# Optimization experiments

Measured on AMD Instinct MI355X. Metric: run time of the kernel, lower is better.

## Reference

```python
import jax, jax.numpy as jnp
import numpy as np

N = 20000      # nodes per snapshot
E = 160000     # edges per snapshot
T = 8          # timesteps
F_IN = 256     # nfeat
HEADS = 4      # GAT heads
C = 128        # nhid_graph (per-head GAT out, concat=False -> mean)
GH = 128       # nhid_gru
NC = 2         # nclass
NEG_SLOPE = 0.2


def setup_inputs() -> dict:
    key = jax.random.key(0)
    ks = jax.random.split(key, 16)
    s = 0.05
    return {
        "graph": jax.random.randint(ks[0], (T, 2, E), 0, N),
        "fts": jax.random.normal(ks[1], (T, N, F_IN), dtype=jnp.float32),
        "time_steps": T,
        # GATConv params (PyG-style): lin weight, att_src/att_dst, bias
        "W_gat": jax.random.normal(ks[2], (F_IN, HEADS * C), dtype=jnp.float32) * s,
        "att_src": jax.random.normal(ks[3], (HEADS, C), dtype=jnp.float32) * s,
        "att_dst": jax.random.normal(ks[4], (HEADS, C), dtype=jnp.float32) * s,
        "b_gat": jax.random.normal(ks[5], (C,), dtype=jnp.float32) * s,
        # GRU params (torch layout: [3H, in], gates order r,z,n)
        "W_ih": jax.random.normal(ks[6], (3 * GH, C), dtype=jnp.float32) * s,
        "W_hh": jax.random.normal(ks[7], (3 * GH, GH), dtype=jnp.float32) * s,
        "b_ih": jax.random.normal(ks[8], (3 * GH,), dtype=jnp.float32) * s,
        "b_hh": jax.random.normal(ks[9], (3 * GH,), dtype=jnp.float32) * s,
        # Attention ('general'): linear_in [H,H] no bias, linear_out [H,2H] no bias
        "W_att_in": jax.random.normal(ks[10], (GH, GH), dtype=jnp.float32) * s,
        "W_att_out": jax.random.normal(ks[11], (GH, 2 * GH), dtype=jnp.float32) * s,
        # final classifier
        "W_cls": jax.random.normal(ks[12], (NC, GH), dtype=jnp.float32) * s,
        "b_cls": jax.random.normal(ks[13], (NC,), dtype=jnp.float32) * s,
    }


def _segment_softmax(logits, seg, num_segments):
    # logits: [E', H], seg: [E'] destination node ids
    m = jax.ops.segment_max(logits, seg, num_segments=num_segments)
    m = jnp.where(jnp.isfinite(m), m, 0.0)
    e = jnp.exp(logits - m[seg])
    s = jax.ops.segment_sum(e, seg, num_segments=num_segments)
    return e / (s[seg] + 1e-16)


def _gat_step(x, edge_index, W_gat, att_src, att_dst, b_gat):
    # PyG GATConv: concat=False (mean over heads), negative_slope=0.2,
    # add_self_loops=True; eval mode so attention dropout is identity.
    n = x.shape[0]
    xw = (x @ W_gat).reshape(n, HEADS, C)                 # [N,H,C]
    loops = jnp.arange(n, dtype=edge_index.dtype)
    src = jnp.concatenate([edge_index[0], loops])         # [E']
    dst = jnp.concatenate([edge_index[1], loops])
    a_src = jnp.einsum('nhc,hc->nh', xw, att_src)         # [N,H]
    a_dst = jnp.einsum('nhc,hc->nh', xw, att_dst)
    alpha = jax.nn.leaky_relu(a_src[src] + a_dst[dst], NEG_SLOPE)  # [E',H]
    alpha = _segment_softmax(alpha, dst, n)
    msg = xw[src] * alpha[..., None]                      # [E',H,C]
    out = jax.ops.segment_sum(msg, dst, num_segments=n)   # [N,H,C]
    return out.mean(axis=1) + b_gat                       # [N,C]


def _gru(y, W_ih, W_hh, b_ih, b_hh):
    # y: [T, N, C]; torch GRU equations, h0 = 0
    n = y.shape[1]
    def step(h, x):
        gi = x @ W_ih.T + b_ih
        gh = h @ W_hh.T + b_hh
        i_r, i_z, i_n = jnp.split(gi, 3, axis=-1)
        h_r, h_z, h_n = jnp.split(gh, 3, axis=-1)
        r = jax.nn.sigmoid(i_r + h_r)
        z = jax.nn.sigmoid(i_z + h_z)
        nn_ = jnp.tanh(i_n + r * h_n)
        h_new = (1.0 - z) * nn_ + z * h
        return h_new, h_new
    h0 = jnp.zeros((n, GH), dtype=y.dtype)
    last, full = jax.lax.scan(step, h0, y)
    return full, last  # [T,N,GH], [N,GH]


def reference(graph, fts, time_steps, W_gat, att_src, att_dst, b_gat,
              W_ih, W_hh, b_ih, b_hh, W_att_in, W_att_out, W_cls, b_cls):
    # per-timestep GAT + leaky_relu(0.2)
    ys = [jax.nn.leaky_relu(
            _gat_step(fts[i], graph[i], W_gat, att_src, att_dst, b_gat),
            NEG_SLOPE)
          for i in range(time_steps)]
    y = jnp.stack(ys)                                     # [T,N,C]
    context, last = _gru(y, W_ih, W_hh, b_ih, b_hh)
    query = last[:, None, :]                              # [N,1,GH]
    context = jnp.transpose(context, (1, 0, 2))           # [N,T,GH]
    # Attention('general')
    q = query @ W_att_in.T                                # [N,1,GH]
    scores = jnp.einsum('nod,ntd->not', q, context)       # [N,1,T]
    w = jax.nn.softmax(scores, axis=-1)
    mix = jnp.einsum('not,ntd->nod', w, context)          # [N,1,GH]
    combined = jnp.concatenate([mix, q], axis=-1)         # [N,1,2GH]
    att_out = jnp.tanh(combined @ W_att_out.T)            # [N,1,GH]
    output = jax.nn.leaky_relu(att_out.reshape(-1, GH), NEG_SLOPE)
    logits = output @ W_cls.T + b_cls                     # [N,NC]
    return jax.nn.log_softmax(logits, axis=1)
```

## Files before the change

kernel.cpp:

```cpp
#include <hip/hip_runtime.h>
#include <hip/hip_bf16.h>
#include <math.h>

#define N_NODES 20000
#define N_EDGES 160000
#define T_STEPS 8
#define F_INC   256
#define HEADS   4
#define CCH     128
#define KC      512
#define GHD     128
#define G3      384
#define SLOPE   0.2f
#define SEG     (N_EDGES + N_NODES)
#define TN      (T_STEPS * N_NODES)
#define SCAN_BLKS ((TN + 1023) / 1024)

typedef unsigned short u16;
typedef __attribute__((ext_vector_type(8))) short bf16x8;
typedef __attribute__((ext_vector_type(4))) float f32x4;

__device__ __forceinline__ float leakyf(float x) { return x > 0.f ? x : SLOPE * x; }
__device__ __forceinline__ float b2f(u16 u) {
  union { unsigned int i; float f; } x; x.i = ((unsigned int)u) << 16; return x.f;
}
__device__ __forceinline__ u16 f2b(float f) {
  union { float f; unsigned int i; } u; u.f = f;
  unsigned int r = u.i + 0x7FFFu + ((u.i >> 16) & 1u);
  return (u16)(r >> 16);
}
__device__ __forceinline__ float sigf(float x) { return 1.f / (1.f + expf(-x)); }

__device__ __forceinline__ void gload16(const void* g, void* l) {
  __builtin_amdgcn_global_load_lds(
      (const __attribute__((address_space(1))) unsigned int*)g,
      (__attribute__((address_space(3))) unsigned int*)l, 16, 0, 0);
}

__device__ __forceinline__ bf16x8 cvt8(f32x4 lo, f32x4 hi) {
  union { unsigned int u[4]; bf16x8 v; } r;
  asm("v_cvt_pk_bf16_f32 %0, %1, %2" : "=v"(r.u[0]) : "v"(lo[0]), "v"(lo[1]));
  asm("v_cvt_pk_bf16_f32 %0, %1, %2" : "=v"(r.u[1]) : "v"(lo[2]), "v"(lo[3]));
  asm("v_cvt_pk_bf16_f32 %0, %1, %2" : "=v"(r.u[2]) : "v"(hi[0]), "v"(hi[1]));
  asm("v_cvt_pk_bf16_f32 %0, %1, %2" : "=v"(r.u[3]) : "v"(hi[2]), "v"(hi[3]));
  return r.v;
}

template <int OBF, int FUSE, int AFP32>
__global__ __launch_bounds__(256) void gemm_bf16(
    const void* __restrict__ Ain, const u16* __restrict__ B,
    const float* __restrict__ bias, void* __restrict__ Cout,
    int M, int K, int Nt, int swz,
    const float* __restrict__ attS, const float* __restrict__ attD,
    float* __restrict__ asrc, float* __restrict__ adst)
{
  __shared__ __align__(16) char AsRaw[128 * 32 * 4];
  __shared__ u16 Bs[128][32];
  __shared__ float s_as[128], s_ad[128];
  float* AsF = (float*)AsRaw;
  u16 (*Asb)[32] = (u16(*)[32])AsRaw;
  const int tid  = threadIdx.x;
  const int wave = tid >> 6, lane = tid & 63;
  const int wr = (wave >> 1) * 64, wc = (wave & 1) * 64;
  int bx = blockIdx.x, by = blockIdx.y;
  if (swz) {
    const int gx = gridDim.x;
    const int nwg = gx * (int)gridDim.y;
    const int lin = by * gx + bx;
    const int q = nwg >> 3, r = nwg & 7;
    const int xcd = lin & 7, idx = lin >> 3;
    const int wg = (xcd < r ? xcd * (q + 1) : r * (q + 1) + (xcd - r) * q) + idx;
    bx = wg % gx; by = wg / gx;
  }
  const int bm = by * 128, bn = bx * 128;
  const int l15 = lane & 15, g = lane >> 4;

  if (FUSE && tid < 128) { s_as[tid] = 0.f; s_ad[tid] = 0.f; }

  const int sr = tid >> 2, sd = tid & 3;
  const int ss = sd ^ ((sr >> 1) & 3);
  const u16* aS0 = 0; const u16* aS1 = 0; u16* lA0 = 0; u16* lA1 = 0;
  const float* aF[4]; float* lAF[4];
  if (AFP32) {
    const float* Af = (const float*)Ain;
    const int row0 = tid >> 3, sd8 = tid & 7;
    const int ss8 = sd8 ^ (row0 & 7);
    #pragma unroll
    for (int p = 0; p < 4; ++p) {
      int row = row0 + p * 32;
      aF[p] = Af + (size_t)min(bm + row, M - 1) * K + ss8 * 4;
      lAF[p] = AsF + (size_t)(p * 256 + (tid & ~63)) * 4;
    }
  } else {
    const u16* Ab = (const u16*)Ain;
    aS0 = Ab + (size_t)min(bm + sr,      M - 1) * K + ss * 8;
    aS1 = Ab + (size_t)min(bm + 64 + sr, M - 1) * K + ss * 8;
    lA0 = (u16*)AsRaw + (size_t)(tid & ~63) * 8;
    lA1 = lA0 + 2048;
  }
  const u16* bS0 = B + (size_t)(bn + sr)      * K + ss * 8;
  const u16* bS1 = B + (size_t)(bn + 64 + sr) * K + ss * 8;
  u16* lB0 = &Bs[0][0] + (size_t)(tid & ~63) * 8;
  u16* lB1 = lB0 + 2048;

  f32x4 acc[4][4];
  #pragma unroll
  for (int m = 0; m < 4; ++m)
    #pragma unroll
    for (int n = 0; n < 4; ++n)
      #pragma unroll
      for (int j = 0; j < 4; ++j) acc[m][n][j] = 0.f;

  const int nK = K >> 5;
  for (int kt = 0; kt < nK; ++kt) {
    const int ko = kt * 32;
    if (AFP32) {
      #pragma unroll
      for (int p = 0; p < 4; ++p) gload16(aF[p] + ko, lAF[p]);
    } else {
      gload16(aS0 + ko, lA0);
      gload16(aS1 + ko, lA1);
    }
    gload16(bS0 + ko, lB0);
    gload16(bS1 + ko, lB1);
    __syncthreads();
    bf16x8 af[4], bfr[4];
    #pragma unroll
    for (int m = 0; m < 4; ++m) {
      int row = wr + m * 16 + l15;
      if (AFP32) {
        int s0 = (2 * g) ^ (row & 7), s1 = (2 * g + 1) ^ (row & 7);
        f32x4 lo = *(const f32x4*)&AsF[row * 32 + s0 * 4];
        f32x4 hi = *(const f32x4*)&AsF[row * 32 + s1 * 4];
        af[m] = cvt8(lo, hi);
      } else {
        af[m] = *(const bf16x8*)&Asb[row][(g ^ ((row >> 1) & 3)) * 8];
      }
      int rowb = wc + m * 16 + l15;
      bfr[m] = *(const bf16x8*)&Bs[rowb][(g ^ ((rowb >> 1) & 3)) * 8];
    }
    #pragma unroll
    for (int m = 0; m < 4; ++m)
      #pragma unroll
      for (int n = 0; n < 4; ++n)
        acc[m][n] = __builtin_amdgcn_mfma_f32_16x16x32_bf16(af[m], bfr[n], acc[m][n], 0, 0, 0);
    __syncthreads();
  }
  if (FUSE != 2) {
    #pragma unroll
    for (int m = 0; m < 4; ++m) {
      int row0 = bm + wr + m * 16 + g * 4;
      #pragma unroll
      for (int n = 0; n < 4; ++n) {
        int col = bn + wc + n * 16 + l15;
        float bv = bias ? bias[col] : 0.f;
        #pragma unroll
        for (int j = 0; j < 4; ++j) {
          int row = row0 + j;
          if (row < M) {
            float v = acc[m][n][j] + bv;
            if (OBF) ((u16*)Cout)[(size_t)row * Nt + col] = f2b(v);
            else     ((float*)Cout)[(size_t)row * Nt + col] = v;
          }
        }
      }
    }
  }
  if (FUSE) {
    float ps[4][4], pd[4][4];
    #pragma unroll
    for (int m = 0; m < 4; ++m)
      #pragma unroll
      for (int j = 0; j < 4; ++j) { ps[m][j] = 0.f; pd[m][j] = 0.f; }
    #pragma unroll
    for (int n = 0; n < 4; ++n) {
      int cl = wc + n * 16 + l15;
      float wsv = attS[bn + cl], wdv = attD[bn + cl];
      #pragma unroll
      for (int m = 0; m < 4; ++m)
        #pragma unroll
        for (int j = 0; j < 4; ++j) {
          float av = acc[m][n][j];
          if (FUSE == 2) av = leakyf(tanhf(av));
          ps[m][j] = fmaf(av, wsv, ps[m][j]);
          pd[m][j] = fmaf(av, wdv, pd[m][j]);
        }
    }
    #pragma unroll
    for (int m = 0; m < 4; ++m)
      #pragma unroll
      for (int j = 0; j < 4; ++j)
        #pragma unroll
        for (int msk = 8; msk >= 1; msk >>= 1) {
          ps[m][j] += __shfl_xor(ps[m][j], msk);
          pd[m][j] += __shfl_xor(pd[m][j], msk);
        }
    if (l15 == 0) {
      #pragma unroll
      for (int m = 0; m < 4; ++m)
        #pragma unroll
        for (int j = 0; j < 4; ++j) {
          atomicAdd(&s_as[wr + m * 16 + g * 4 + j], ps[m][j]);
          atomicAdd(&s_ad[wr + m * 16 + g * 4 + j], pd[m][j]);
        }
    }
    __syncthreads();
    if (tid < 128) {
      int row = bm + tid;
      if (row < M) {
        if (FUSE == 1) {
          int h = bn >> 7;
          asrc[(size_t)row * 4 + h] = s_as[tid];
          adst[(size_t)row * 4 + h] = s_ad[tid];
        } else {
          float l0 = s_as[tid] + bias[0];
          float l1 = s_ad[tid] + bias[1];
          float mx = fmaxf(l0, l1);
          float lse = mx + logf(expf(l0 - mx) + expf(l1 - mx));
          asrc[(size_t)row * 2 + 0] = l0 - lse;
          asrc[(size_t)row * 2 + 1] = l1 - lse;
        }
      }
    }
  }
}

__global__ void convert_weights(const float* __restrict__ w_ih, const float* __restrict__ w_hh,
                                const float* __restrict__ w_in, const float* __restrict__ w_out,
                                u16* __restrict__ wihb, u16* __restrict__ whhb,
                                u16* __restrict__ winb, u16* __restrict__ woutb)
{
  int i = blockIdx.x * 256 + threadIdx.x;
  const float* src; u16* dst; int base;
  if      (i < 6144)  { src = w_ih;  dst = wihb;  base = i; }
  else if (i < 12288) { src = w_hh;  dst = whhb;  base = i - 6144; }
  else if (i < 14336) { src = w_in;  dst = winb;  base = i - 12288; }
  else                { src = w_out; dst = woutb; base = i - 14336; }
  int o = base * 8;
  float4 v0 = *(const float4*)(src + o);
  float4 v1 = *(const float4*)(src + o + 4);
  bf16x8 ov;
  ov[0] = (short)f2b(v0.x); ov[1] = (short)f2b(v0.y);
  ov[2] = (short)f2b(v0.z); ov[3] = (short)f2b(v0.w);
  ov[4] = (short)f2b(v1.x); ov[5] = (short)f2b(v1.y);
  ov[6] = (short)f2b(v1.z); ov[7] = (short)f2b(v1.w);
  *(bf16x8*)(dst + o) = ov;
}

__global__ void conv_transpose_wgat(const float* __restrict__ src, u16* __restrict__ dst) {
  int idx = blockIdx.x * 256 + threadIdx.x;
  if (idx >= KC * F_INC) return;
  int n = idx >> 8, k = idx & 255;
  dst[(size_t)n * F_INC + k] = f2b(src[(size_t)k * KC + n]);
}

__global__ void count_kernel(const int* __restrict__ graph, int* __restrict__ counts) {
  int e = blockIdx.x * 256 + threadIdx.x;
  int t = blockIdx.y;
  if (e < N_EDGES) {
    int d = graph[(size_t)t * 2 * N_EDGES + N_EDGES + e];
    atomicAdd(&counts[t * N_NODES + d], 1);
  }
}

__global__ __launch_bounds__(1024) void scanA(
    const int* __restrict__ counts, int* __restrict__ offs, int* __restrict__ bsums)
{
  const int tid = threadIdx.x, lane = tid & 63, w = tid >> 6;
  __shared__ int s_wt[16];
  int i = blockIdx.x * 1024 + tid;
  int v = (i < TN) ? (counts[i] + 1) : 0;
  int x = v;
  #pragma unroll
  for (int d = 1; d < 64; d <<= 1) {
    int nvl = __shfl_up(x, d, 64);
    if (lane >= d) x += nvl;
  }
  if (lane == 63) s_wt[w] = x;
  __syncthreads();
  if (tid < 16) {
    int y = s_wt[tid];
    #pragma unroll
    for (int d = 1; d < 16; d <<= 1) {
      int nvl = __shfl_up(y, d, 64);
      if (tid >= d) y += nvl;
    }
    s_wt[tid] = y;
  }
  __syncthreads();
  int wbase = (w > 0) ? s_wt[w - 1] : 0;
  if (i < TN) offs[i] = wbase + x - v;
  if (tid == 1023) bsums[blockIdx.x] = s_wt[15];
}

__global__ void scanB(int* __restrict__ bsums, int* __restrict__ offs) {
  const int lane = threadIdx.x;
  int carry = 0;
  for (int base = 0; base < 192; base += 64) {
    int idx = base + lane;
    int v = (idx < SCAN_BLKS) ? bsums[idx] : 0;
    int x = v;
    #pragma unroll
    for (int d = 1; d < 64; d <<= 1) {
      int nvl = __shfl_up(x, d, 64);
      if (lane >= d) x += nvl;
    }
    if (idx < SCAN_BLKS) bsums[idx] = carry + x - v;
    carry += __shfl(x, 63);
  }
  if (lane == 0) offs[TN] = carry;
}

__global__ __launch_bounds__(1024) void scanC(int* __restrict__ offs, const int* __restrict__ bsums) {
  int i = blockIdx.x * 1024 + threadIdx.x;
  if (i < TN) offs[i] += bsums[blockIdx.x];
}

__global__ void scatter_kernel(const int* __restrict__ graph, const int* __restrict__ offs,
                               int* __restrict__ cursor, int* __restrict__ ssrc)
{
  int i = blockIdx.x * 256 + threadIdx.x;
  int t = blockIdx.y;
  if (i >= SEG) return;
  int s, d;
  if (i < N_EDGES) {
    s = graph[(size_t)t * 2 * N_EDGES + i];
    d = graph[(size_t)t * 2 * N_EDGES + N_EDGES + i];
  } else {
    s = d = i - N_EDGES;
  }
  int pos = offs[t * N_NODES + d] + atomicAdd(&cursor[t * N_NODES + d], 1);
  ssrc[pos] = s;
}

__global__ __launch_bounds__(256) void aggregate_kernel(
    const u16* __restrict__ xw, const float* __restrict__ a_src,
    const float* __restrict__ a_dst, const float* __restrict__ b_gat,
    const int* __restrict__ offs, const int* __restrict__ ssrc,
    u16* __restrict__ yout)
{
  const int wv = threadIdx.x >> 6, lane = threadIdx.x & 63;
  const int nd = blockIdx.x * 4 + wv;
  const int t  = blockIdx.y;
  const int ob = t * N_NODES + nd;
  const int beg = offs[ob], end = offs[ob + 1];
  const size_t rowbase = (size_t)t * N_NODES;
  const int he   = lane & 3;
  const int eidx = lane >> 2;
  const int hl   = lane >> 4;
  const float advh = a_dst[(rowbase + nd) * 4 + he];

  float m = -INFINITY, ssum = 0.f;
  float acc[8] = {0.f,0.f,0.f,0.f,0.f,0.f,0.f,0.f};

#define FMA8(W, X)                                                        \
    { float _w = (W);                                                     \
      acc[0] = fmaf(_w, __uint_as_float((unsigned)(X).x << 16), acc[0]);  \
      acc[1] = fmaf(_w, __uint_as_float((unsigned)(X).x & 0xffff0000u), acc[1]); \
      acc[2] = fmaf(_w, __uint_as_float((unsigned)(X).y << 16), acc[2]);  \
      acc[3] = fmaf(_w, __uint_as_float((unsigned)(X).y & 0xffff0000u), acc[3]); \
      acc[4] = fmaf(_w, __uint_as_float((unsigned)(X).z << 16), acc[4]);  \
      acc[5] = fmaf(_w, __uint_as_float((unsigned)(X).z & 0xffff0000u), acc[5]); \
      acc[6] = fmaf(_w, __uint_as_float((unsigned)(X).w << 16), acc[6]);  \
      acc[7] = fmaf(_w, __uint_as_float((unsigned)(X).w & 0xffff0000u), acc[7]); }
#define LDE(SVAR) (*(const int4*)&xw[(rowbase + (SVAR)) * KC + lane * 8])

  for (int base = beg; base < end; base += 16) {
    const int cnt = min(16, end - base);
    const int e = base + eidx;
    const int sidx = (e < end) ? ssrc[e] : ssrc[base];
    const float av = a_src[(rowbase + sidx) * 4 + he];
    const float a = (eidx < cnt) ? leakyf(av + advh) : -INFINITY;
    float cm = a;
    cm = fmaxf(cm, __shfl_xor(cm, 4));
    cm = fmaxf(cm, __shfl_xor(cm, 8));
    cm = fmaxf(cm, __shfl_xor(cm, 16));
    cm = fmaxf(cm, __shfl_xor(cm, 32));
    const float nm = fmaxf(m, cm);
    const float sc = expf(m - nm);
    const float w = expf(a - nm);
    float ts = w;
    ts += __shfl_xor(ts, 4);
    ts += __shfl_xor(ts, 8);
    ts += __shfl_xor(ts, 16);
    ts += __shfl_xor(ts, 32);
    ssum = ssum * sc + ts;
    m = nm;
    const float schl = __shfl(sc, hl);
    #pragma unroll
    for (int k = 0; k < 8; ++k) acc[k] *= schl;

    const int cpad = (cnt + 3) & ~3;
    int b4 = 0;
    for (; b4 + 8 <= cpad; b4 += 8) {
      const int s0 = __shfl(sidx, (b4 + 0) << 2);
      const int s1 = __shfl(sidx, (b4 + 1) << 2);
      const int s2 = __shfl(sidx, (b4 + 2) << 2);
      const int s3 = __shfl(sidx, (b4 + 3) << 2);
      const int s4 = __shfl(sidx, (b4 + 4) << 2);
      const int s5 = __shfl(sidx, (b4 + 5) << 2);
      const int s6 = __shfl(sidx, (b4 + 6) << 2);
      const int s7 = __shfl(sidx, (b4 + 7) << 2);
      const int4 x0 = LDE(s0); const int4 x1 = LDE(s1);
      const int4 x2 = LDE(s2); const int4 x3 = LDE(s3);
      const int4 x4 = LDE(s4); const int4 x5 = LDE(s5);
      const int4 x6 = LDE(s6); const int4 x7 = LDE(s7);
      const float w0 = __shfl(w, ((b4 + 0) << 2) + hl);
      const float w1 = __shfl(w, ((b4 + 1) << 2) + hl);
      const float w2 = __shfl(w, ((b4 + 2) << 2) + hl);
      const float w3 = __shfl(w, ((b4 + 3) << 2) + hl);
      const float w4 = __shfl(w, ((b4 + 4) << 2) + hl);
      const float w5 = __shfl(w, ((b4 + 5) << 2) + hl);
      const float w6 = __shfl(w, ((b4 + 6) << 2) + hl);
      const float w7 = __shfl(w, ((b4 + 7) << 2) + hl);
      FMA8(w0, x0); FMA8(w1, x1); FMA8(w2, x2); FMA8(w3, x3);
      FMA8(w4, x4); FMA8(w5, x5); FMA8(w6, x6); FMA8(w7, x7);
    }
    if (b4 < cpad) {
      const int s0 = __shfl(sidx, (b4 + 0) << 2);
      const int s1 = __shfl(sidx, (b4 + 1) << 2);
      const int s2 = __shfl(sidx, (b4 + 2) << 2);
      const int s3 = __shfl(sidx, (b4 + 3) << 2);
      const int4 x0 = LDE(s0); const int4 x1 = LDE(s1);
      const int4 x2 = LDE(s2); const int4 x3 = LDE(s3);
      const float w0 = __shfl(w, ((b4 + 0) << 2) + hl);
      const float w1 = __shfl(w, ((b4 + 1) << 2) + hl);
      const float w2 = __shfl(w, ((b4 + 2) << 2) + hl);
      const float w3 = __shfl(w, ((b4 + 3) << 2) + hl);
      FMA8(w0, x0); FMA8(w1, x1); FMA8(w2, x2); FMA8(w3, x3);
    }
  }
#undef LDE
#undef FMA8

  const float sh = __shfl(ssum, hl);
  const float inv = 1.f / (sh + 1e-16f);
  #pragma unroll
  for (int k = 0; k < 8; ++k) {
    acc[k] *= inv;
    acc[k] += __shfl_xor(acc[k], 16);
    acc[k] += __shfl_xor(acc[k], 32);
  }
  if (lane < 16) {
    bf16x8 ov;
    #pragma unroll
    for (int k = 0; k < 8; ++k) {
      float v = acc[k] * 0.25f + b_gat[lane * 8 + k];
      ov[k] = (short)f2b(leakyf(v));
    }
    *(bf16x8*)&yout[(rowbase + nd) * GHD + lane * 8] = ov;
  }
}

__global__ __launch_bounds__(256) void gru_seq(
    const u16* __restrict__ Whh, const float* __restrict__ b_hh,
    const u16* __restrict__ giall, u16* __restrict__ ctx)
{
  __shared__ u16 hA[32][128];
  __shared__ u16 reg2[12288];
  u16 (*Bs)[32] = (u16(*)[32])reg2;
  const int tid = threadIdx.x, lane = tid & 63, wv = tid >> 6;
  const int l15 = lane & 15, g = lane >> 4;
  const int bm = blockIdx.x * 32;

  const int sr = tid >> 2, sd = tid & 3;
  const int ssb = sd ^ ((sr >> 1) & 3);
  const u16* bS[6]; u16* lB[6];
  #pragma unroll
  for (int p = 0; p < 6; ++p) {
    bS[p] = Whh + (size_t)(sr + p * 64) * GHD + ssb * 8;
    lB[p] = reg2 + (size_t)(p * 256 + (tid & ~63)) * 8;
  }
  float bbv[6];
  #pragma unroll
  for (int n = 0; n < 6; ++n) bbv[n] = b_hh[wv * 96 + n * 16 + l15];

  const int cr = tid >> 3;
  const int cg = (tid & 7) * 8;
  const int grow = bm + cr;
  const size_t gb = (size_t)grow * G3;
  const size_t cb = (size_t)grow * GHD;
  float hp[2][8];

  #pragma unroll
  for (int q = 0; q < 2; ++q) {
    const int c0 = cg + q * 64;
    bf16x8 ir8 = *(const bf16x8*)&giall[gb + c0];
    bf16x8 iz8 = *(const bf16x8*)&giall[gb + 128 + c0];
    bf16x8 in8 = *(const bf16x8*)&giall[gb + 256 + c0];
    float4 br0 = *(const float4*)&b_hh[c0];       float4 br1 = *(const float4*)&b_hh[c0 + 4];
    float4 bz0 = *(const float4*)&b_hh[128 + c0]; float4 bz1 = *(const float4*)&b_hh[128 + c0 + 4];
    float4 bn0 = *(const float4*)&b_hh[256 + c0]; float4 bn1 = *(const float4*)&b_hh[256 + c0 + 4];
    float bhr[8] = {br0.x, br0.y, br0.z, br0.w, br1.x, br1.y, br1.z, br1.w};
    float bhz[8] = {bz0.x, bz0.y, bz0.z, bz0.w, bz1.x, bz1.y, bz1.z, bz1.w};
    float bhn[8] = {bn0.x, bn0.y, bn0.z, bn0.w, bn1.x, bn1.y, bn1.z, bn1.w};
    bf16x8 hv;
    #pragma unroll
    for (int k = 0; k < 8; ++k) {
      float rr = sigf(b2f((u16)ir8[k]) + bhr[k]);
      float zz = sigf(b2f((u16)iz8[k]) + bhz[k]);
      float nn = tanhf(b2f((u16)in8[k]) + rr * bhn[k]);
      float h = (1.f - zz) * nn;
      hp[q][k] = h;
      hv[k] = (short)f2b(h);
    }
    const int sl = (c0 >> 3) ^ (cr & 7);
    *(bf16x8*)&hA[cr][sl * 8] = hv;
    *(bf16x8*)&ctx[cb + c0] = hv;
  }
  __syncthreads();

  for (int t = 1; t < T_STEPS; ++t) {
    const u16* gi_t = giall + (size_t)t * N_NODES * G3;
    u16* ctx_t = ctx + (size_t)t * N_NODES * GHD;
    f32x4 acc[2][6];
    #pragma unroll
    for (int m = 0; m < 2; ++m)
      #pragma unroll
      for (int n = 0; n < 6; ++n)
        #pragma unroll
        for (int j = 0; j < 4; ++j) acc[m][n][j] = 0.f;

    #pragma unroll
    for (int kt = 0; kt < 4; ++kt) {
      const int ko = kt * 32;
      #pragma unroll
      for (int p = 0; p < 6; ++p) gload16(bS[p] + ko, lB[p]);
      __syncthreads();
      bf16x8 af[2], bfr[6];
      #pragma unroll
      for (int m = 0; m < 2; ++m) {
        int row = m * 16 + l15;
        int sl = (kt * 4 + g) ^ (row & 7);
        af[m] = *(const bf16x8*)&hA[row][sl * 8];
      }
      #pragma unroll
      for (int n = 0; n < 6; ++n) {
        int rowb = wv * 96 + n * 16 + l15;
        bfr[n] = *(const bf16x8*)&Bs[rowb][(g ^ ((rowb >> 1) & 3)) * 8];
      }
      #pragma unroll
      for (int m = 0; m < 2; ++m)
        #pragma unroll
        for (int n = 0; n < 6; ++n)
          acc[m][n] = __builtin_amdgcn_mfma_f32_16x16x32_bf16(af[m], bfr[n], acc[m][n], 0, 0, 0);
      __syncthreads();
    }
    #pragma unroll
    for (int m = 0; m < 2; ++m)
      #pragma unroll
      for (int n = 0; n < 6; ++n) {
        int c = wv * 96 + n * 16 + l15;
        #pragma unroll
        for (int j = 0; j < 4; ++j) {
          int r = m * 16 + g * 4 + j;
          reg2[r * 384 + (((c >> 3) ^ (r & 7)) << 3) + (c & 7)] = f2b(acc[m][n][j] + bbv[n]);
        }
      }
    __syncthreads();
    #pragma unroll
    for (int q = 0; q < 2; ++q) {
      const int c0 = cg + q * 64;
      const int sl0 = ((c0 >> 3) ^ (cr & 7));
      const int sl1 = (((128 + c0) >> 3) ^ (cr & 7));
      const int sl2 = (((256 + c0) >> 3) ^ (cr & 7));
      bf16x8 hr8 = *(bf16x8*)&reg2[cr * 384 + sl0 * 8];
      bf16x8 hz8 = *(bf16x8*)&reg2[cr * 384 + sl1 * 8];
      bf16x8 hn8 = *(bf16x8*)&reg2[cr * 384 + sl2 * 8];
      bf16x8 ir8 = *(const bf16x8*)&gi_t[gb + c0];
      bf16x8 iz8 = *(const bf16x8*)&gi_t[gb + 128 + c0];
      bf16x8 in8 = *(const bf16x8*)&gi_t[gb + 256 + c0];
      bf16x8 hv;
      #pragma unroll
      for (int k = 0; k < 8; ++k) {
        float rr = sigf(b2f((u16)ir8[k]) + b2f((u16)hr8[k]));
        float zz = sigf(b2f((u16)iz8[k]) + b2f((u16)hz8[k]));
        float nn = tanhf(b2f((u16)in8[k]) + rr * b2f((u16)hn8[k]));
        float h = (1.f - zz) * nn + zz * hp[q][k];
        hp[q][k] = h;
        hv[k] = (short)f2b(h);
      }
      const int slh = (c0 >> 3) ^ (cr & 7);
      *(bf16x8*)&hA[cr][slh * 8] = hv;
      *(bf16x8*)&ctx_t[cb + c0] = hv;
    }
    __syncthreads();
  }
}

__global__ __launch_bounds__(256) void attn_mid(
    const u16* __restrict__ ctx, const float* __restrict__ q,
    u16* __restrict__ comb)
{
  const int node = blockIdx.x * 4 + (threadIdx.x >> 6);
  const int lane = threadIdx.x & 63;
  if (node >= N_NODES) return;
  const float q0 = q[(size_t)node * GHD + lane];
  const float q1 = q[(size_t)node * GHD + 64 + lane];
  float c0[T_STEPS], c1[T_STEPS], w[T_STEPS];
  float mx = -1e30f;
  #pragma unroll
  for (int t = 0; t < T_STEPS; ++t) {
    const u16* cr = ctx + ((size_t)t * N_NODES + node) * GHD;
    c0[t] = b2f(cr[lane]); c1[t] = b2f(cr[64 + lane]);
    float p = q0 * c0[t] + q1 * c1[t];
    #pragma unroll
    for (int m = 32; m >= 1; m >>= 1) p += __shfl_xor(p, m);
    w[t] = p;
    mx = fmaxf(mx, p);
  }
  float s = 0.f;
  #pragma unroll
  for (int t = 0; t < T_STEPS; ++t) { w[t] = expf(w[t] - mx); s += w[t]; }
  const float inv = 1.f / s;
  float m0 = 0.f, m1 = 0.f;
  #pragma unroll
  for (int t = 0; t < T_STEPS; ++t) { m0 = fmaf(w[t], c0[t], m0); m1 = fmaf(w[t], c1[t], m1); }
  m0 *= inv; m1 *= inv;
  u16* cb = comb + (size_t)node * 2 * GHD;
  cb[lane]       = f2b(m0);
  cb[64 + lane]  = f2b(m1);
  cb[128 + lane] = f2b(q0);
  cb[192 + lane] = f2b(q1);
}

extern "C" void kernel_launch(void* const* d_in, const int* in_sizes, int n_in,
                              void* d_out, int out_size, void* d_ws, size_t ws_size,
                              hipStream_t stream)
{
  const int*   graph     = (const int*)  d_in[0];
  const float* fts       = (const float*)d_in[1];
  const float* W_gat     = (const float*)d_in[3];
  const float* att_src   = (const float*)d_in[4];
  const float* att_dst   = (const float*)d_in[5];
  const float* b_gat     = (const float*)d_in[6];
  const float* W_ih      = (const float*)d_in[7];
  const float* W_hh      = (const float*)d_in[8];
  const float* b_ih      = (const float*)d_in[9];
  const float* b_hh      = (const float*)d_in[10];
  const float* W_att_in  = (const float*)d_in[11];
  const float* W_att_out = (const float*)d_in[12];
  const float* W_cls     = (const float*)d_in[13];
  const float* b_cls     = (const float*)d_in[14];
  float* out = (float*)d_out;

  char* ws = (char*)d_ws;
  size_t off = 0;
  auto alloc = [&](size_t bytes) {
    void* p = ws + off;
    off = (off + bytes + 255) & ~(size_t)255;
    return p;
  };
  const size_t NT = (size_t)TN;
  u16*   wgatT = (u16*)alloc((size_t)KC * F_INC * 2);
  u16*   wihb  = (u16*)alloc((size_t)G3 * GHD * 2);
  u16*   whhb  = (u16*)alloc((size_t)G3 * GHD * 2);
  u16*   winb  = (u16*)alloc((size_t)GHD * GHD * 2);
  u16*   woutb = (u16*)alloc((size_t)GHD * 2 * GHD * 2);
  u16*   xw    = (u16*)alloc(NT * KC * 2);
  float* asrc  = (float*)alloc(NT * 4 * 4);
  float* adst  = (float*)alloc(NT * 4 * 4);
  u16*   yall  = (u16*)alloc(NT * GHD * 2);
  u16*   giall = (u16*)alloc(NT * G3 * 2);
  u16*   ctx   = (u16*)alloc(NT * GHD * 2);
  float* qf    = (float*)alloc((size_t)N_NODES * GHD * 4);
  u16*   comb  = (u16*)alloc((size_t)N_NODES * 2 * GHD * 2);
  int* counts  = (int*)alloc((size_t)2 * TN * 4);
  int* cursor  = counts + TN;
  int* offs    = (int*)alloc((size_t)(TN + 1) * 4);
  int* bsums   = (int*)alloc((size_t)256 * 4);
  int* ssrc    = (int*)alloc((size_t)T_STEPS * SEG * 4);

  conv_transpose_wgat<<<dim3((KC * F_INC + 255) / 256), 256, 0, stream>>>(W_gat, wgatT);
  convert_weights<<<dim3(72), 256, 0, stream>>>(W_ih, W_hh, W_att_in, W_att_out,
                                                wihb, whhb, winb, woutb);

  hipMemsetAsync(counts, 0, (size_t)2 * TN * 4, stream);
  count_kernel<<<dim3(N_EDGES / 256, T_STEPS), 256, 0, stream>>>(graph, counts);
  scanA<<<dim3(SCAN_BLKS), 1024, 0, stream>>>(counts, offs, bsums);
  scanB<<<dim3(1), 64, 0, stream>>>(bsums, offs);
  scanC<<<dim3(SCAN_BLKS), 1024, 0, stream>>>(offs, bsums);
  scatter_kernel<<<dim3((SEG + 255) / 256, T_STEPS), 256, 0, stream>>>(graph, offs, cursor, ssrc);

  gemm_bf16<1, 1, 1><<<dim3(KC / 128, (int)(NT / 128)), 256, 0, stream>>>(
      fts, wgatT, nullptr, xw, (int)NT, F_INC, KC, 1, att_src, att_dst, asrc, adst);

  aggregate_kernel<<<dim3(N_NODES / 4, T_STEPS), 256, 0, stream>>>(
      xw, asrc, adst, b_gat, offs, ssrc, yall);

  gemm_bf16<1, 0, 0><<<dim3(G3 / 128, (int)(NT / 128)), 256, 0, stream>>>(
      yall, wihb, b_ih, giall, (int)NT, GHD, G3, 1, nullptr, nullptr, nullptr, nullptr);

  gru_seq<<<dim3(N_NODES / 32), 256, 0, stream>>>(whhb, b_hh, giall, ctx);

  gemm_bf16<0, 0, 0><<<dim3(1, (N_NODES + 127) / 128), 256, 0, stream>>>(
      ctx + (size_t)(T_STEPS - 1) * N_NODES * GHD, winb, nullptr, qf,
      N_NODES, GHD, GHD, 0, nullptr, nullptr, nullptr, nullptr);
  attn_mid<<<dim3(N_NODES / 4), 256, 0, stream>>>(ctx, qf, comb);
  gemm_bf16<0, 2, 0><<<dim3(1, (N_NODES + 127) / 128), 256, 0, stream>>>(
      comb, woutb, b_cls, nullptr, N_NODES, 2 * GHD, GHD, 0,
      W_cls, W_cls + GHD, out, nullptr);
}
```

Measured before the change: 724.6 us.

## Fuse query projection into GRU kernel, merge weight conversions, pack aggregate FMAs

Computes the attention query projection (last hidden state times W_att_in) inside the GRU kernel epilogue, using the final hidden tile still held in LDS. This removes a separate GEMM launch and the reload of the last context slice, and stores q as bf16 instead of fp32. The two weight conversion kernels are merged into one launch. The aggregate kernel's accumulators become float2 vectors so the compiler can emit packed FMA. The bf16 q adds slight rounding, and the fused epilogue reuses shared buffers, so correctness depends on that LDS state being valid.

```diff
diff --git a/kernel.cpp b/kernel.cpp
--- a/kernel.cpp
+++ b/kernel.cpp
@@ -19,6 +19,7 @@
 typedef unsigned short u16;
 typedef __attribute__((ext_vector_type(8))) short bf16x8;
 typedef __attribute__((ext_vector_type(4))) float f32x4;
+typedef __attribute__((ext_vector_type(2))) float f32x2;
 
 __device__ __forceinline__ float leakyf(float x) { return x > 0.f ? x : SLOPE * x; }
 __device__ __forceinline__ float b2f(u16 u) {
@@ -225,12 +226,21 @@
   }
 }
 
-__global__ void convert_weights(const float* __restrict__ w_ih, const float* __restrict__ w_hh,
-                                const float* __restrict__ w_in, const float* __restrict__ w_out,
-                                u16* __restrict__ wihb, u16* __restrict__ whhb,
-                                u16* __restrict__ winb, u16* __restrict__ woutb)
+__global__ void convert_all(const float* __restrict__ w_gat,
+                            const float* __restrict__ w_ih, const float* __restrict__ w_hh,
+                            const float* __restrict__ w_in, const float* __restrict__ w_out,
+                            u16* __restrict__ wgatT,
+                            u16* __restrict__ wihb, u16* __restrict__ whhb,
+                            u16* __restrict__ winb, u16* __restrict__ woutb)
 {
-  int i = blockIdx.x * 256 + threadIdx.x;
+  int b = blockIdx.x;
+  if (b < 512) {
+    int idx = b * 256 + threadIdx.x;
+    int n = idx >> 8, k = idx & 255;
+    wgatT[(size_t)n * F_INC + k] = f2b(w_gat[(size_t)k * KC + n]);
+    return;
+  }
+  int i = (b - 512) * 256 + threadIdx.x;
   const float* src; u16* dst; int base;
   if      (i < 6144)  { src = w_ih;  dst = wihb;  base = i; }
   else if (i < 12288) { src = w_hh;  dst = whhb;  base = i - 6144; }
@@ -245,13 +255,6 @@
   ov[4] = (short)f2b(v1.x); ov[5] = (short)f2b(v1.y);
   ov[6] = (short)f2b(v1.z); ov[7] = (short)f2b(v1.w);
   *(bf16x8*)(dst + o) = ov;
-}
-
-__global__ void conv_transpose_wgat(const float* __restrict__ src, u16* __restrict__ dst) {
-  int idx = blockIdx.x * 256 + threadIdx.x;
-  if (idx >= KC * F_INC) return;
-  int n = idx >> 8, k = idx & 255;
-  dst[(size_t)n * F_INC + k] = f2b(src[(size_t)k * KC + n]);
 }
 
 __global__ void count_kernel(const int* __restrict__ graph, int* __restrict__ counts) {
@@ -351,18 +354,25 @@
   const float advh = a_dst[(rowbase + nd) * 4 + he];
 
   float m = -INFINITY, ssum = 0.f;
-  float acc[8] = {0.f,0.f,0.f,0.f,0.f,0.f,0.f,0.f};
+  f32x2 acc2[4];
+  #pragma unroll
+  for (int j = 0; j < 4; ++j) { acc2[j][0] = 0.f; acc2[j][1] = 0.f; }
 
 #define FMA8(W, X)                                                        \
-    { float _w = (W);                                                     \
-      acc[0] = fmaf(_w, __uint_as_float((unsigned)(X).x << 16), acc[0]);  \
-      acc[1] = fmaf(_w, __uint_as_float((unsigned)(X).x & 0xffff0000u), acc[1]); \
-      acc[2] = fmaf(_w, __uint_as_float((unsigned)(X).y << 16), acc[2]);  \
-      acc[3] = fmaf(_w, __uint_as_float((unsigned)(X).y & 0xffff0000u), acc[3]); \
-      acc[4] = fmaf(_w, __uint_as_float((unsigned)(X).z << 16), acc[4]);  \
-      acc[5] = fmaf(_w, __uint_as_float((unsigned)(X).z & 0xffff0000u), acc[5]); \
-      acc[6] = fmaf(_w, __uint_as_float((unsigned)(X).w << 16), acc[6]);  \
-      acc[7] = fmaf(_w, __uint_as_float((unsigned)(X).w & 0xffff0000u), acc[7]); }
+    { f32x2 _w2; _w2[0] = (W); _w2[1] = _w2[0];                           \
+      f32x2 _v;                                                           \
+      _v[0] = __uint_as_float((unsigned)(X).x << 16);                     \
+      _v[1] = __uint_as_float((unsigned)(X).x & 0xffff0000u);             \
+      acc2[0] += _w2 * _v;                                                \
+      _v[0] = __uint_as_float((unsigned)(X).y << 16);                     \
+      _v[1] = __uint_as_float((unsigned)(X).y & 0xffff0000u);             \
+      acc2[1] += _w2 * _v;                                                \
+      _v[0] = __uint_as_float((unsigned)(X).z << 16);                     \
+      _v[1] = __uint_as_float((unsigned)(X).z & 0xffff0000u);             \
+      acc2[2] += _w2 * _v;                                                \
+      _v[0] = __uint_as_float((unsigned)(X).w << 16);                     \
+      _v[1] = __uint_as_float((unsigned)(X).w & 0xffff0000u);             \
+      acc2[3] += _w2 * _v; }
 #define LDE(SVAR) (*(const int4*)&xw[(rowbase + (SVAR)) * KC + lane * 8])
 
   for (int base = beg; base < end; base += 16) {
@@ -386,9 +396,12 @@
     ts += __shfl_xor(ts, 32);
     ssum = ssum * sc + ts;
     m = nm;
-    const float schl = __shfl(sc, hl);
-    #pragma unroll
-    for (int k = 0; k < 8; ++k) acc[k] *= schl;
+    {
+      const float schl = __shfl(sc, hl);
+      f32x2 sc2; sc2[0] = schl; sc2[1] = schl;
+      #pragma unroll
+      for (int j = 0; j < 4; ++j) acc2[j] *= sc2;
+    }
 
     const int cpad = (cnt + 3) & ~3;
     int b4 = 0;
@@ -435,9 +448,10 @@
 
   const float sh = __shfl(ssum, hl);
   const float inv = 1.f / (sh + 1e-16f);
+  float acc[8];
   #pragma unroll
   for (int k = 0; k < 8; ++k) {
-    acc[k] *= inv;
+    acc[k] = acc2[k >> 1][k & 1] * inv;
     acc[k] += __shfl_xor(acc[k], 16);
     acc[k] += __shfl_xor(acc[k], 32);
   }
@@ -453,8 +467,9 @@
 }
 
 __global__ __launch_bounds__(256) void gru_seq(
-    const u16* __restrict__ Whh, const float* __restrict__ b_hh,
-    const u16* __restrict__ giall, u16* __restrict__ ctx)
+    const u16* __restrict__ Whh, const u16* __restrict__ Win,
+    const float* __restrict__ b_hh, const u16* __restrict__ giall,
+    u16* __restrict__ ctx, u16* __restrict__ qb)
 {
   __shared__ u16 hA[32][128];
   __shared__ u16 reg2[12288];
@@ -586,17 +601,70 @@
     }
     __syncthreads();
   }
+
+  {
+    const u16* qS[2]; u16* lQ[2];
+    #pragma unroll
+    for (int p = 0; p < 2; ++p) {
+      qS[p] = Win + (size_t)(sr + p * 64) * GHD + ssb * 8;
+      lQ[p] = reg2 + (size_t)(p * 256 + (tid & ~63)) * 8;
+    }
+    f32x4 accq[2][2];
+    #pragma unroll
+    for (int m = 0; m < 2; ++m)
+      #pragma unroll
+      for (int n = 0; n < 2; ++n)
+        #pragma unroll
+        for (int j = 0; j < 4; ++j) accq[m][n][j] = 0.f;
+
+    #pragma unroll
+    for (int kt = 0; kt < 4; ++kt) {
+      const int ko = kt * 32;
+      #pragma unroll
+      for (int p = 0; p < 2; ++p) gload16(qS[p] + ko, lQ[p]);
+      __syncthreads();
+      bf16x8 af[2], bq[2];
+      #pragma unroll
+      for (int m = 0; m < 2; ++m) {
+        int row = m * 16 + l15;
+        int sl = (kt * 4 + g) ^ (row & 7);
+        af[m] = *(const bf16x8*)&hA[row][sl * 8];
+      }
+      #pragma unroll
+      for (int n = 0; n < 2; ++n) {
+        int rowb = wv * 32 + n * 16 + l15;
+        bq[n] = *(const bf16x8*)&Bs[rowb][(g ^ ((rowb >> 1) & 3)) * 8];
+      }
+      #pragma unroll
+      for (int m = 0; m < 2; ++m)
+        #pragma unroll
+        for (int n = 0; n < 2; ++n)
+          accq[m][n] = __builtin_amdgcn_mfma_f32_16x16x32_bf16(af[m], bq[n], accq[m][n], 0, 0, 0);
+      __syncthreads();
+    }
+    #pragma unroll
+    for (int m = 0; m < 2; ++m) {
+      int row0 = bm + m * 16 + g * 4;
+      #pragma unroll
+      for (int n = 0; n < 2; ++n) {
+        int col = wv * 32 + n * 16 + l15;
+        #pragma unroll
+        for (int j = 0; j < 4; ++j)
+          qb[(size_t)(row0 + j) * GHD + col] = f2b(accq[m][n][j]);
+      }
+    }
+  }
 }
 
 __global__ __launch_bounds__(256) void attn_mid(
-    const u16* __restrict__ ctx, const float* __restrict__ q,
+    const u16* __restrict__ ctx, const u16* __restrict__ qb,
     u16* __restrict__ comb)
 {
   const int node = blockIdx.x * 4 + (threadIdx.x >> 6);
   const int lane = threadIdx.x & 63;
   if (node >= N_NODES) return;
-  const float q0 = q[(size_t)node * GHD + lane];
-  const float q1 = q[(size_t)node * GHD + 64 + lane];
+  const float q0 = b2f(qb[(size_t)node * GHD + lane]);
+  const float q1 = b2f(qb[(size_t)node * GHD + 64 + lane]);
   float c0[T_STEPS], c1[T_STEPS], w[T_STEPS];
   float mx = -1e30f;
   #pragma unroll
@@ -620,8 +688,8 @@
   u16* cb = comb + (size_t)node * 2 * GHD;
   cb[lane]       = f2b(m0);
   cb[64 + lane]  = f2b(m1);
-  cb[128 + lane] = f2b(q0);
-  cb[192 + lane] = f2b(q1);
+  cb[128 + lane] = qb[(size_t)node * GHD + lane];
+  cb[192 + lane] = qb[(size_t)node * GHD + 64 + lane];
 }
 
 extern "C" void kernel_launch(void* const* d_in, const int* in_sizes, int n_in,
@@ -663,7 +731,7 @@
   u16*   yall  = (u16*)alloc(NT * GHD * 2);
   u16*   giall = (u16*)alloc(NT * G3 * 2);
   u16*   ctx   = (u16*)alloc(NT * GHD * 2);
-  float* qf    = (float*)alloc((size_t)N_NODES * GHD * 4);
+  u16*   qb    = (u16*)alloc((size_t)N_NODES * GHD * 2);
   u16*   comb  = (u16*)alloc((size_t)N_NODES * 2 * GHD * 2);
   int* counts  = (int*)alloc((size_t)2 * TN * 4);
   int* cursor  = counts + TN;
@@ -671,9 +739,8 @@
   int* bsums   = (int*)alloc((size_t)256 * 4);
   int* ssrc    = (int*)alloc((size_t)T_STEPS * SEG * 4);
 
-  conv_transpose_wgat<<<dim3((KC * F_INC + 255) / 256), 256, 0, stream>>>(W_gat, wgatT);
-  convert_weights<<<dim3(72), 256, 0, stream>>>(W_ih, W_hh, W_att_in, W_att_out,
-                                                wihb, whhb, winb, woutb);
+  convert_all<<<dim3(584), 256, 0, stream>>>(W_gat, W_ih, W_hh, W_att_in, W_att_out,
+                                             wgatT, wihb, whhb, winb, woutb);
 
   hipMemsetAsync(counts, 0, (size_t)2 * TN * 4, stream);
   count_kernel<<<dim3(N_EDGES / 256, T_STEPS), 256, 0, stream>>>(graph, counts);
@@ -691,12 +758,9 @@
   gemm_bf16<1, 0, 0><<<dim3(G3 / 128, (int)(NT / 128)), 256, 0, stream>>>(
       yall, wihb, b_ih, giall, (int)NT, GHD, G3, 1, nullptr, nullptr, nullptr, nullptr);
 
-  gru_seq<<<dim3(N_NODES / 32), 256, 0, stream>>>(whhb, b_hh, giall, ctx);
-
-  gemm_bf16<0, 0, 0><<<dim3(1, (N_NODES + 127) / 128), 256, 0, stream>>>(
-      ctx + (size_t)(T_STEPS - 1) * N_NODES * GHD, winb, nullptr, qf,
-      N_NODES, GHD, GHD, 0, nullptr, nullptr, nullptr, nullptr);
-  attn_mid<<<dim3(N_NODES / 4), 256, 0, stream>>>(ctx, qf, comb);
+  gru_seq<<<dim3(N_NODES / 32), 256, 0, stream>>>(whhb, winb, b_hh, giall, ctx, qb);
+
+  attn_mid<<<dim3(N_NODES / 4), 256, 0, stream>>>(ctx, qb, comb);
   gemm_bf16<0, 2, 0><<<dim3(1, (N_NODES + 127) / 128), 256, 0, stream>>>(
       comb, woutb, b_cls, nullptr, N_NODES, 2 * GHD, GHD, 0,
       W_cls, W_cls + GHD, out, nullptr);
```

After: 712.8 us. Within noise of the previous version (-1.6%).
